# Optimization experiments

Hardware: AMD Instinct MI355X
Metric: run time of the kernel (lower is better)

Reference implementation:

```python
import jax, jax.numpy as jnp
import numpy as np

N_NODE = 100000
N_REL = 32
EMB = 128
N_HOP = 2
K = 16  # n_neighbor
B = 2048
EPS = 1e-8


def setup_inputs() -> dict:
    key = jax.random.key(0)
    ks = jax.random.split(key, 12)
    inp = {
        'node': jax.random.randint(ks[0], (B,), 0, N_NODE),
        'relation': jax.random.randint(ks[1], (B,), 0, N_REL),
        'adj_node': jax.random.randint(ks[2], (N_NODE, K), 0, N_NODE),
        'adj_rela': jax.random.randint(ks[3], (N_NODE, K), 0, N_REL),
        # learned parameters
        'node_table': jax.random.normal(ks[4], (N_NODE, EMB), jnp.float32) * 0.1,
        'rela_table': jax.random.normal(ks[5], (N_REL, EMB), jnp.float32) * 0.1,
        'proj_table': jax.random.normal(ks[6], (N_REL, EMB), jnp.float32) * 0.1,  # DistMult diag projection
        'W0': jax.random.normal(ks[7], (EMB, EMB), jnp.float32) * (1.0 / np.sqrt(EMB)),
        'b0': jnp.zeros((EMB,), jnp.float32),
        'W1': jax.random.normal(ks[8], (EMB, EMB), jnp.float32) * (1.0 / np.sqrt(EMB)),
        'b1': jnp.zeros((EMB,), jnp.float32),
    }
    return inp


def _abs_cos(a, b):
    # a: [B,n,K,E], b: [B,1,1,E] -> [B,n,K]
    num = jnp.sum(a * b, axis=-1)
    den = jnp.linalg.norm(a, axis=-1) * jnp.linalg.norm(b, axis=-1) + EPS
    return jnp.abs(num / den)


def _pgra_forward(node, relation, adj_node, adj_rela,
                  node_table, rela_table, proj_table, W0, b0, W1, b1):
    bsz = node.shape[0]
    # --- get_neighbors: multi-hop adjacency gathers ---
    e0 = node[:, None]                               # [B,1]
    e1 = adj_node[e0].reshape(bsz, -1)               # [B,K]
    e2 = adj_node[e1].reshape(bsz, -1)               # [B,K^2]
    r0 = adj_rela[e0].reshape(bsz, -1)               # [B,K]
    r1 = adj_rela[e1].reshape(bsz, -1)               # [B,K^2]

    target = rela_table[relation]                    # [B,E]
    proj = proj_table[relation]                      # [B,E] DistMult diagonal

    def pemb(idx):  # relation-aware projected node embedding
        return node_table[idx] * proj[:, None, :]

    ev = [pemb(e0), pemb(e1), pemb(e2)]              # [B,1,E],[B,K,E],[B,K^2,E]
    rv = [rela_table[r0], rela_table[r1]]
    Ws = [(W0, b0), (W1, b1)]

    def aggregate(i, nb_v, nb_r):
        # nb_v, nb_r: [B,n,K,E]
        score = _abs_cos(nb_r, target[:, None, None, :])   # [B,n,K]
        att = jax.nn.softmax(score, axis=-1)
        out = jnp.einsum('bnk,bnke->bne', att, nb_v)       # attention-weighted agg
        W, b = Ws[i]
        return jnp.tanh(out @ W + b)

    for i in range(N_HOP):
        nxt = []
        for hop in range(N_HOP - i):
            nb_v = ev[hop + 1].reshape(bsz, -1, K, EMB)
            nb_r = rv[hop].reshape(bsz, -1, K, EMB)
            nxt.append(aggregate(i, nb_v, nb_r))
        ev = nxt
    return ev[0].reshape(bsz, EMB)


def reference(node, relation, adj_node, adj_rela,
              node_table, rela_table, proj_table, W0, b0, W1, b1):
    return _pgra_forward(node, relation, adj_node, adj_rela,
                         node_table, rela_table, proj_table, W0, b0, W1, b1)
```

## Files before the change

### kernel.cpp

```cpp
#include <hip/hip_runtime.h>

#define EMB 128
#define KN 16
#define NREL 32

__device__ __forceinline__ float fast_tanh(float x) {
    const float z = __expf(2.0f * x);
    return 1.0f - __fdividef(2.0f, z + 1.0f);
}

__global__ __launch_bounds__(256) void pgra_costab_k(const float* __restrict__ rela,
                                                     float* __restrict__ costab) {
    const int pair = blockIdx.x * 4 + (threadIdx.x >> 6);
    const int lane = threadIdx.x & 63;
    const int r = pair >> 5, c = pair & 31;
    const float2 av = ((const float2*)(rela + (size_t)r * EMB))[lane];
    const float2 bv = ((const float2*)(rela + (size_t)c * EMB))[lane];
    float dot = av.x * bv.x + av.y * bv.y;
    float na  = av.x * av.x + av.y * av.y;
    float nb  = bv.x * bv.x + bv.y * bv.y;
    #pragma unroll
    for (int off = 32; off > 0; off >>= 1) {
        dot += __shfl_xor(dot, off);
        na  += __shfl_xor(na,  off);
        nb  += __shfl_xor(nb,  off);
    }
    if (lane == 0)
        costab[pair] = fabsf(dot / (sqrtf(na) * sqrtf(nb) + 1e-8f));
}

__global__ __launch_bounds__(256) void pgra_gather5(
    const int* __restrict__ node, const int* __restrict__ relation,
    const int* __restrict__ adj_node, const int* __restrict__ adj_rela,
    const float* __restrict__ node_table, const float* __restrict__ proj_table,
    const float* __restrict__ costab, float* __restrict__ agg, int npair)
{
    const int p = blockIdx.x * 4 + (threadIdx.x >> 6);
    if (p >= npair) return;
    const int lane = threadIdx.x & 63;
    const int b = p >> 4, j = p & 15;

    const int n0  = node[b];
    const int rel = relation[b];
    const int n1  = adj_node[n0 * KN + j];

    const int4* n2p = (const int4*)(adj_node + (size_t)n1 * KN);
    const int4* r1p = (const int4*)(adj_rela + (size_t)n1 * KN);
    const int4 nn0 = n2p[0], nn1 = n2p[1], nn2 = n2p[2], nn3 = n2p[3];
    const int4 rr0 = r1p[0], rr1 = r1p[1], rr2 = r1p[2], rr3 = r1p[3];

    float2 v0,v1,v2,v3,v4,v5,v6,v7,v8,v9,v10,v11,v12,v13,v14,v15;
    v0  = ((const float2*)(node_table + (size_t)nn0.x * EMB))[lane];
    v1  = ((const float2*)(node_table + (size_t)nn0.y * EMB))[lane];
    v2  = ((const float2*)(node_table + (size_t)nn0.z * EMB))[lane];
    v3  = ((const float2*)(node_table + (size_t)nn0.w * EMB))[lane];
    v4  = ((const float2*)(node_table + (size_t)nn1.x * EMB))[lane];
    v5  = ((const float2*)(node_table + (size_t)nn1.y * EMB))[lane];
    v6  = ((const float2*)(node_table + (size_t)nn1.z * EMB))[lane];
    v7  = ((const float2*)(node_table + (size_t)nn1.w * EMB))[lane];
    v8  = ((const float2*)(node_table + (size_t)nn2.x * EMB))[lane];
    v9  = ((const float2*)(node_table + (size_t)nn2.y * EMB))[lane];
    v10 = ((const float2*)(node_table + (size_t)nn2.z * EMB))[lane];
    v11 = ((const float2*)(node_table + (size_t)nn2.w * EMB))[lane];
    v12 = ((const float2*)(node_table + (size_t)nn3.x * EMB))[lane];
    v13 = ((const float2*)(node_table + (size_t)nn3.y * EMB))[lane];
    v14 = ((const float2*)(node_table + (size_t)nn3.z * EMB))[lane];
    v15 = ((const float2*)(node_table + (size_t)nn3.w * EMB))[lane];

    float sc[KN];
    sc[0]  = costab[rr0.x * NREL + rel]; sc[1]  = costab[rr0.y * NREL + rel];
    sc[2]  = costab[rr0.z * NREL + rel]; sc[3]  = costab[rr0.w * NREL + rel];
    sc[4]  = costab[rr1.x * NREL + rel]; sc[5]  = costab[rr1.y * NREL + rel];
    sc[6]  = costab[rr1.z * NREL + rel]; sc[7]  = costab[rr1.w * NREL + rel];
    sc[8]  = costab[rr2.x * NREL + rel]; sc[9]  = costab[rr2.y * NREL + rel];
    sc[10] = costab[rr2.z * NREL + rel]; sc[11] = costab[rr2.w * NREL + rel];
    sc[12] = costab[rr3.x * NREL + rel]; sc[13] = costab[rr3.y * NREL + rel];
    sc[14] = costab[rr3.z * NREL + rel]; sc[15] = costab[rr3.w * NREL + rel];

    float m = sc[0];
    #pragma unroll
    for (int k = 1; k < KN; ++k) m = fmaxf(m, sc[k]);
    float sum = 0.f;
    #pragma unroll
    for (int k = 0; k < KN; ++k) { sc[k] = __expf(sc[k] - m); sum += sc[k]; }
    const float inv = __fdividef(1.f, sum);

    float ax = 0.f, ay = 0.f;
    ax = fmaf(sc[0],  v0.x,  ax); ay = fmaf(sc[0],  v0.y,  ay);
    ax = fmaf(sc[1],  v1.x,  ax); ay = fmaf(sc[1],  v1.y,  ay);
    ax = fmaf(sc[2],  v2.x,  ax); ay = fmaf(sc[2],  v2.y,  ay);
    ax = fmaf(sc[3],  v3.x,  ax); ay = fmaf(sc[3],  v3.y,  ay);
    ax = fmaf(sc[4],  v4.x,  ax); ay = fmaf(sc[4],  v4.y,  ay);
    ax = fmaf(sc[5],  v5.x,  ax); ay = fmaf(sc[5],  v5.y,  ay);
    ax = fmaf(sc[6],  v6.x,  ax); ay = fmaf(sc[6],  v6.y,  ay);
    ax = fmaf(sc[7],  v7.x,  ax); ay = fmaf(sc[7],  v7.y,  ay);
    ax = fmaf(sc[8],  v8.x,  ax); ay = fmaf(sc[8],  v8.y,  ay);
    ax = fmaf(sc[9],  v9.x,  ax); ay = fmaf(sc[9],  v9.y,  ay);
    ax = fmaf(sc[10], v10.x, ax); ay = fmaf(sc[10], v10.y, ay);
    ax = fmaf(sc[11], v11.x, ax); ay = fmaf(sc[11], v11.y, ay);
    ax = fmaf(sc[12], v12.x, ax); ay = fmaf(sc[12], v12.y, ay);
    ax = fmaf(sc[13], v13.x, ax); ay = fmaf(sc[13], v13.y, ay);
    ax = fmaf(sc[14], v14.x, ax); ay = fmaf(sc[14], v14.y, ay);
    ax = fmaf(sc[15], v15.x, ax); ay = fmaf(sc[15], v15.y, ay);

    const float2 pj = ((const float2*)(proj_table + (size_t)rel * EMB))[lane];
    float2 o;
    o.x = ax * inv * pj.x;
    o.y = ay * inv * pj.y;
    ((float2*)(agg + (size_t)p * EMB))[lane] = o;
}

__global__ __launch_bounds__(256) void pgra_tail4(
    const int* __restrict__ node, const int* __restrict__ relation,
    const int* __restrict__ adj_rela, const float* __restrict__ agg,
    const float* __restrict__ W0, const float* __restrict__ b0,
    const float* __restrict__ W1, const float* __restrict__ b1,
    const float* __restrict__ costab, float* __restrict__ out)
{
    const int blk  = blockIdx.x;
    const int tid  = threadIdx.x;
    const int wave = tid >> 6;
    const int lane = tid & 63;
    const int b    = blk * 4 + wave;

    __shared__ float s_agg[4][KN][EMB];
    __shared__ float s_fin[4][EMB];

    {
        const float4* ap = (const float4*)(agg + (size_t)blk * 4 * KN * EMB);
        float4* sp = (float4*)&s_agg[0][0][0];
        #pragma unroll
        for (int q = 0; q < 8; ++q) sp[tid + 256 * q] = ap[tid + 256 * q];
    }
    __syncthreads();

    const int n0  = node[b];
    const int rel = relation[b];

    float acc0[KN], acc1[KN];
    const float bias0 = b0[lane];
    const float bias1 = b0[lane + 64];
    #pragma unroll
    for (int k = 0; k < KN; ++k) { acc0[k] = bias0; acc1[k] = bias1; }

    for (int ee4 = 0; ee4 < EMB / 4; ++ee4) {
        const int row = 4 * ee4;
        float w0a[4], w0b[4];
        #pragma unroll
        for (int r = 0; r < 4; ++r) {
            w0a[r] = W0[(row + r) * EMB + lane];
            w0b[r] = W0[(row + r) * EMB + lane + 64];
        }
        #pragma unroll
        for (int k = 0; k < KN; ++k) {
            const float4 a = *(const float4*)&s_agg[wave][k][row];
            acc0[k] = fmaf(a.x, w0a[0], fmaf(a.y, w0a[1], fmaf(a.z, w0a[2], fmaf(a.w, w0a[3], acc0[k]))));
            acc1[k] = fmaf(a.x, w0b[0], fmaf(a.y, w0b[1], fmaf(a.z, w0b[2], fmaf(a.w, w0b[3], acc1[k]))));
        }
    }

    float sc0[KN];
    float m = -1e30f;
    {
        const int4* r0p = (const int4*)(adj_rela + (size_t)n0 * KN);
        #pragma unroll
        for (int q = 0; q < 4; ++q) {
            const int4 rr = r0p[q];
            sc0[4*q+0] = costab[rr.x * NREL + rel];
            sc0[4*q+1] = costab[rr.y * NREL + rel];
            sc0[4*q+2] = costab[rr.z * NREL + rel];
            sc0[4*q+3] = costab[rr.w * NREL + rel];
        }
    }
    #pragma unroll
    for (int k = 0; k < KN; ++k) m = fmaxf(m, sc0[k]);
    float sum = 0.f;
    #pragma unroll
    for (int k = 0; k < KN; ++k) { sc0[k] = __expf(sc0[k] - m); sum += sc0[k]; }
    const float inv = __fdividef(1.f, sum);
    float fin0 = 0.f, fin1 = 0.f;
    #pragma unroll
    for (int k = 0; k < KN; ++k) {
        const float w = sc0[k] * inv;
        fin0 = fmaf(w, fast_tanh(acc0[k]), fin0);
        fin1 = fmaf(w, fast_tanh(acc1[k]), fin1);
    }
    s_fin[wave][lane]      = fin0;
    s_fin[wave][lane + 64] = fin1;
    __syncthreads();

    float o0 = b1[lane], o1 = b1[lane + 64];
    for (int ee4 = 0; ee4 < EMB / 4; ++ee4) {
        const int row = 4 * ee4;
        const float4 f = *(const float4*)&s_fin[wave][row];
        float w1a[4], w1b[4];
        #pragma unroll
        for (int r = 0; r < 4; ++r) {
            w1a[r] = W1[(row + r) * EMB + lane];
            w1b[r] = W1[(row + r) * EMB + lane + 64];
        }
        o0 = fmaf(f.x, w1a[0], fmaf(f.y, w1a[1], fmaf(f.z, w1a[2], fmaf(f.w, w1a[3], o0))));
        o1 = fmaf(f.x, w1b[0], fmaf(f.y, w1b[1], fmaf(f.z, w1b[2], fmaf(f.w, w1b[3], o1))));
    }
    out[(size_t)b * EMB + lane]      = fast_tanh(o0);
    out[(size_t)b * EMB + lane + 64] = fast_tanh(o1);
}

__global__ __launch_bounds__(1024) void pgra_fused(
    const int* __restrict__ node, const int* __restrict__ relation,
    const int* __restrict__ adj_node, const int* __restrict__ adj_rela,
    const float* __restrict__ node_table, const float* __restrict__ proj_table,
    const float* __restrict__ W0, const float* __restrict__ b0,
    const float* __restrict__ W1, const float* __restrict__ b1,
    const float* __restrict__ costab, float* __restrict__ out)
{
    const int b    = blockIdx.x;
    const int tid  = threadIdx.x;
    const int wave = tid >> 6;
    const int lane = tid & 63;

    __shared__ float s_agg[KN][EMB];
    __shared__ float s_part[2][EMB];
    __shared__ float s_fin[EMB];

    const int n0  = node[b];
    const int rel = relation[b];

    {
        const int j  = wave;
        const int n1 = adj_node[n0 * KN + j];
        const int4* n2p = (const int4*)(adj_node + (size_t)n1 * KN);
        const int4* r1p = (const int4*)(adj_rela + (size_t)n1 * KN);
        int   n2[KN];
        float sc[KN];
        #pragma unroll
        for (int q = 0; q < 4; ++q) {
            const int4 nn = n2p[q];
            const int4 rr = r1p[q];
            n2[4*q+0] = nn.x; n2[4*q+1] = nn.y; n2[4*q+2] = nn.z; n2[4*q+3] = nn.w;
            sc[4*q+0] = costab[rr.x * NREL + rel];
            sc[4*q+1] = costab[rr.y * NREL + rel];
            sc[4*q+2] = costab[rr.z * NREL + rel];
            sc[4*q+3] = costab[rr.w * NREL + rel];
        }
        float m = sc[0];
        #pragma unroll
        for (int k = 1; k < KN; ++k) m = fmaxf(m, sc[k]);
        float sum = 0.f;
        #pragma unroll
        for (int k = 0; k < KN; ++k) { sc[k] = __expf(sc[k] - m); sum += sc[k]; }
        const float inv = 1.f / sum;
        float ax = 0.f, ay = 0.f;
        #pragma unroll
        for (int k = 0; k < KN; ++k) {
            const float2 v = ((const float2*)(node_table + (size_t)n2[k] * EMB))[lane];
            ax = fmaf(sc[k], v.x, ax);
            ay = fmaf(sc[k], v.y, ay);
        }
        const float2 pj = ((const float2*)(proj_table + (size_t)rel * EMB))[lane];
        s_agg[j][2*lane]   = ax * inv * pj.x;
        s_agg[j][2*lane+1] = ay * inv * pj.y;
    }
    __syncthreads();

    if (tid < 256) {
        const int e  = tid & 127;
        const int g  = tid >> 7;
        const int jg = g * 8;
        float acc[8];
        const float bias = b0[e];
        #pragma unroll
        for (int q = 0; q < 8; ++q) acc[q] = bias;
        for (int ee4 = 0; ee4 < EMB / 4; ++ee4) {
            const float w0v = W0[(4 * ee4 + 0) * EMB + e];
            const float w1v = W0[(4 * ee4 + 1) * EMB + e];
            const float w2v = W0[(4 * ee4 + 2) * EMB + e];
            const float w3v = W0[(4 * ee4 + 3) * EMB + e];
            #pragma unroll
            for (int q = 0; q < 8; ++q) {
                const float4 a = *(const float4*)&s_agg[jg + q][4 * ee4];
                acc[q] = fmaf(a.x, w0v, fmaf(a.y, w1v, fmaf(a.z, w2v, fmaf(a.w, w3v, acc[q]))));
            }
        }
        float sc0[KN];
        float m = -1e30f;
        #pragma unroll
        for (int k = 0; k < KN; ++k) {
            sc0[k] = costab[adj_rela[n0 * KN + k] * NREL + rel];
            m = fmaxf(m, sc0[k]);
        }
        float sum = 0.f;
        #pragma unroll
        for (int k = 0; k < KN; ++k) { sc0[k] = __expf(sc0[k] - m); sum += sc0[k]; }
        const float inv = 1.f / sum;
        float part = 0.f;
        #pragma unroll
        for (int q = 0; q < 8; ++q)
            part = fmaf(sc0[jg + q] * inv, fast_tanh(acc[q]), part);
        s_part[g][e] = part;
    }
    __syncthreads();

    if (tid < EMB) s_fin[tid] = s_part[0][tid] + s_part[1][tid];
    __syncthreads();

    if (tid < EMB) {
        float acc = b1[tid];
        for (int ee = 0; ee < EMB; ++ee) acc = fmaf(s_fin[ee], W1[ee * EMB + tid], acc);
        out[(size_t)b * EMB + tid] = fast_tanh(acc);
    }
}

extern "C" void kernel_launch(void* const* d_in, const int* in_sizes, int n_in,
                              void* d_out, int out_size, void* d_ws, size_t ws_size,
                              hipStream_t stream) {
    const int*   node       = (const int*)d_in[0];
    const int*   relation   = (const int*)d_in[1];
    const int*   adj_node   = (const int*)d_in[2];
    const int*   adj_rela   = (const int*)d_in[3];
    const float* node_table = (const float*)d_in[4];
    const float* rela_table = (const float*)d_in[5];
    const float* proj_table = (const float*)d_in[6];
    const float* W0         = (const float*)d_in[7];
    const float* b0         = (const float*)d_in[8];
    const float* W1         = (const float*)d_in[9];
    const float* b1         = (const float*)d_in[10];
    float* outp = (float*)d_out;
    const int B = in_sizes[0];

    float* costab = (float*)d_ws;
    float* agg    = (float*)d_ws + 1024;
    const size_t need = (size_t)(1024 + (size_t)B * KN * EMB) * sizeof(float);

    hipLaunchKernelGGL(pgra_costab_k, dim3(NREL * NREL / 4), dim3(256), 0, stream,
                       rela_table, costab);

    if (ws_size >= need && (B % 4) == 0) {
        const int npair = B * KN;
        hipLaunchKernelGGL(pgra_gather5, dim3((npair + 3) / 4), dim3(256), 0, stream,
                           node, relation, adj_node, adj_rela,
                           node_table, proj_table, costab, agg, npair);
        hipLaunchKernelGGL(pgra_tail4, dim3(B / 4), dim3(256), 0, stream,
                           node, relation, adj_rela, agg,
                           W0, b0, W1, b1, costab, outp);
    } else {
        hipLaunchKernelGGL(pgra_fused, dim3(B), dim3(1024), 0, stream,
                           node, relation, adj_node, adj_rela,
                           node_table, proj_table, W0, b0, W1, b1, costab, outp);
    }
}
```

Measured before the change: 81.50 us.

## Retile tail GEMV to float4 column blocks with half-wave neighbor split

The tail kernel now gives each lane four consecutive output columns loaded as float4 from W0/W1, and splits the 16 neighbors (and the W1 reduction rows) between the two half-waves. The half-wave partial results are combined with cross-lane shuffles. This cuts scalar global weight loads and register pressure, and overlaps the attention-score gather with the shared-memory fill by moving the first barrier later. The gather kernel gains a scheduling barrier so all node-table loads are issued before the score math. The cost is the extra shuffles and half of the lanes sitting idle at the final store.

```diff
diff --git a/kernel.cpp b/kernel.cpp
--- a/kernel.cpp
+++ b/kernel.cpp
@@ -7,6 +7,12 @@
 __device__ __forceinline__ float fast_tanh(float x) {
     const float z = __expf(2.0f * x);
     return 1.0f - __fdividef(2.0f, z + 1.0f);
+}
+
+__device__ __forceinline__ float4 fma4(float s, float4 v, float4 a) {
+    a.x = fmaf(s, v.x, a.x); a.y = fmaf(s, v.y, a.y);
+    a.z = fmaf(s, v.z, a.z); a.w = fmaf(s, v.w, a.w);
+    return a;
 }
 
 __global__ __launch_bounds__(256) void pgra_costab_k(const float* __restrict__ rela,
@@ -29,7 +35,7 @@
         costab[pair] = fabsf(dot / (sqrtf(na) * sqrtf(nb) + 1e-8f));
 }
 
-__global__ __launch_bounds__(256) void pgra_gather5(
+__global__ __launch_bounds__(256) void pgra_gather6(
     const int* __restrict__ node, const int* __restrict__ relation,
     const int* __restrict__ adj_node, const int* __restrict__ adj_rela,
     const float* __restrict__ node_table, const float* __restrict__ proj_table,
@@ -66,6 +72,7 @@
     v13 = ((const float2*)(node_table + (size_t)nn3.y * EMB))[lane];
     v14 = ((const float2*)(node_table + (size_t)nn3.z * EMB))[lane];
     v15 = ((const float2*)(node_table + (size_t)nn3.w * EMB))[lane];
+    __builtin_amdgcn_sched_barrier(0);
 
     float sc[KN];
     sc[0]  = costab[rr0.x * NREL + rel]; sc[1]  = costab[rr0.y * NREL + rel];
@@ -110,7 +117,7 @@
     ((float2*)(agg + (size_t)p * EMB))[lane] = o;
 }
 
-__global__ __launch_bounds__(256) void pgra_tail4(
+__global__ __launch_bounds__(256) void pgra_tail11(
     const int* __restrict__ node, const int* __restrict__ relation,
     const int* __restrict__ adj_rela, const float* __restrict__ agg,
     const float* __restrict__ W0, const float* __restrict__ b0,
@@ -121,6 +128,8 @@
     const int tid  = threadIdx.x;
     const int wave = tid >> 6;
     const int lane = tid & 63;
+    const int h    = lane >> 5;
+    const int c    = lane & 31;
     const int b    = blk * 4 + wave;
 
     __shared__ float s_agg[4][KN][EMB];
@@ -132,35 +141,11 @@
         #pragma unroll
         for (int q = 0; q < 8; ++q) sp[tid + 256 * q] = ap[tid + 256 * q];
     }
-    __syncthreads();
 
     const int n0  = node[b];
     const int rel = relation[b];
 
-    float acc0[KN], acc1[KN];
-    const float bias0 = b0[lane];
-    const float bias1 = b0[lane + 64];
-    #pragma unroll
-    for (int k = 0; k < KN; ++k) { acc0[k] = bias0; acc1[k] = bias1; }
-
-    for (int ee4 = 0; ee4 < EMB / 4; ++ee4) {
-        const int row = 4 * ee4;
-        float w0a[4], w0b[4];
-        #pragma unroll
-        for (int r = 0; r < 4; ++r) {
-            w0a[r] = W0[(row + r) * EMB + lane];
-            w0b[r] = W0[(row + r) * EMB + lane + 64];
-        }
-        #pragma unroll
-        for (int k = 0; k < KN; ++k) {
-            const float4 a = *(const float4*)&s_agg[wave][k][row];
-            acc0[k] = fmaf(a.x, w0a[0], fmaf(a.y, w0a[1], fmaf(a.z, w0a[2], fmaf(a.w, w0a[3], acc0[k]))));
-            acc1[k] = fmaf(a.x, w0b[0], fmaf(a.y, w0b[1], fmaf(a.z, w0b[2], fmaf(a.w, w0b[3], acc1[k]))));
-        }
-    }
-
     float sc0[KN];
-    float m = -1e30f;
     {
         const int4* r0p = (const int4*)(adj_rela + (size_t)n0 * KN);
         #pragma unroll
@@ -172,38 +157,75 @@
             sc0[4*q+3] = costab[rr.w * NREL + rel];
         }
     }
-    #pragma unroll
-    for (int k = 0; k < KN; ++k) m = fmaxf(m, sc0[k]);
+    float m = sc0[0];
+    #pragma unroll
+    for (int k = 1; k < KN; ++k) m = fmaxf(m, sc0[k]);
     float sum = 0.f;
     #pragma unroll
     for (int k = 0; k < KN; ++k) { sc0[k] = __expf(sc0[k] - m); sum += sc0[k]; }
     const float inv = __fdividef(1.f, sum);
-    float fin0 = 0.f, fin1 = 0.f;
-    #pragma unroll
-    for (int k = 0; k < KN; ++k) {
-        const float w = sc0[k] * inv;
-        fin0 = fmaf(w, fast_tanh(acc0[k]), fin0);
-        fin1 = fmaf(w, fast_tanh(acc1[k]), fin1);
-    }
-    s_fin[wave][lane]      = fin0;
-    s_fin[wave][lane + 64] = fin1;
-    __syncthreads();
-
-    float o0 = b1[lane], o1 = b1[lane + 64];
-    for (int ee4 = 0; ee4 < EMB / 4; ++ee4) {
+
+    __syncthreads();
+
+    float4 acc[8];
+    const float4 bias = *(const float4*)&b0[4 * c];
+    #pragma unroll
+    for (int kk = 0; kk < 8; ++kk) acc[kk] = bias;
+
+    for (int ee4 = 0; ee4 < 32; ++ee4) {
         const int row = 4 * ee4;
+        float4 w0q[4];
+        #pragma unroll
+        for (int r = 0; r < 4; ++r)
+            w0q[r] = *(const float4*)&W0[(row + r) * EMB + 4 * c];
+        #pragma unroll
+        for (int kk = 0; kk < 8; ++kk) {
+            const float4 a = *(const float4*)&s_agg[wave][8 * h + kk][row];
+            acc[kk] = fma4(a.x, w0q[0], fma4(a.y, w0q[1],
+                      fma4(a.z, w0q[2], fma4(a.w, w0q[3], acc[kk]))));
+        }
+    }
+
+    float4 part = make_float4(0.f, 0.f, 0.f, 0.f);
+    #pragma unroll
+    for (int kk = 0; kk < 8; ++kk) {
+        const float w = sc0[8 * h + kk] * inv;
+        part.x = fmaf(w, fast_tanh(acc[kk].x), part.x);
+        part.y = fmaf(w, fast_tanh(acc[kk].y), part.y);
+        part.z = fmaf(w, fast_tanh(acc[kk].z), part.z);
+        part.w = fmaf(w, fast_tanh(acc[kk].w), part.w);
+    }
+    part.x += __shfl_xor(part.x, 32);
+    part.y += __shfl_xor(part.y, 32);
+    part.z += __shfl_xor(part.z, 32);
+    part.w += __shfl_xor(part.w, 32);
+    if (h == 0) *(float4*)&s_fin[wave][4 * c] = part;
+    __syncthreads();
+
+    float4 o = make_float4(0.f, 0.f, 0.f, 0.f);
+    for (int i = 0; i < 16; ++i) {
+        const int row = 64 * h + 4 * i;
         const float4 f = *(const float4*)&s_fin[wave][row];
-        float w1a[4], w1b[4];
-        #pragma unroll
-        for (int r = 0; r < 4; ++r) {
-            w1a[r] = W1[(row + r) * EMB + lane];
-            w1b[r] = W1[(row + r) * EMB + lane + 64];
-        }
-        o0 = fmaf(f.x, w1a[0], fmaf(f.y, w1a[1], fmaf(f.z, w1a[2], fmaf(f.w, w1a[3], o0))));
-        o1 = fmaf(f.x, w1b[0], fmaf(f.y, w1b[1], fmaf(f.z, w1b[2], fmaf(f.w, w1b[3], o1))));
-    }
-    out[(size_t)b * EMB + lane]      = fast_tanh(o0);
-    out[(size_t)b * EMB + lane + 64] = fast_tanh(o1);
+        float4 w1q[4];
+        #pragma unroll
+        for (int r = 0; r < 4; ++r)
+            w1q[r] = *(const float4*)&W1[(row + r) * EMB + 4 * c];
+        o = fma4(f.x, w1q[0], fma4(f.y, w1q[1],
+            fma4(f.z, w1q[2], fma4(f.w, w1q[3], o))));
+    }
+    o.x += __shfl_xor(o.x, 32);
+    o.y += __shfl_xor(o.y, 32);
+    o.z += __shfl_xor(o.z, 32);
+    o.w += __shfl_xor(o.w, 32);
+    if (h == 0) {
+        const float4 bb = *(const float4*)&b1[4 * c];
+        float4 r;
+        r.x = fast_tanh(o.x + bb.x);
+        r.y = fast_tanh(o.y + bb.y);
+        r.z = fast_tanh(o.z + bb.z);
+        r.w = fast_tanh(o.w + bb.w);
+        *(float4*)&out[(size_t)b * EMB + 4 * c] = r;
+    }
 }
 
 __global__ __launch_bounds__(1024) void pgra_fused(
@@ -337,10 +359,10 @@
 
     if (ws_size >= need && (B % 4) == 0) {
         const int npair = B * KN;
-        hipLaunchKernelGGL(pgra_gather5, dim3((npair + 3) / 4), dim3(256), 0, stream,
+        hipLaunchKernelGGL(pgra_gather6, dim3((npair + 3) / 4), dim3(256), 0, stream,
                            node, relation, adj_node, adj_rela,
                            node_table, proj_table, costab, agg, npair);
-        hipLaunchKernelGGL(pgra_tail4, dim3(B / 4), dim3(256), 0, stream,
+        hipLaunchKernelGGL(pgra_tail11, dim3(B / 4), dim3(256), 0, stream,
                            node, relation, adj_rela, agg,
                            W0, b0, W1, b1, costab, outp);
     } else {
```

Result: faster. 73.79 us (-9.5%).
